# Optimization experiments

Hardware: AMD Instinct MI355X
Metric: run time of the kernel (lower is better)

The kernel has to match this reference:

```python
import jax, jax.numpy as jnp
import numpy as np

N = 80000      # points (voxels)
M = 2048       # windows
C = 128        # d_model
H = 8          # heads
D = C // H     # head_dim = 16
B = 2          # batch size
HB, WB = 32, 32  # BEV window grid shape


def setup_inputs() -> dict:
    key = jax.random.key(0)
    k1, k2, k3, k4 = jax.random.split(key, 4)
    x = jax.random.normal(k1, (N, C), dtype=jnp.float32)
    Wqkv = jax.random.normal(k2, (3 * C, C), dtype=jnp.float32) * 0.05
    Wproj = jax.random.normal(k3, (C, C), dtype=jnp.float32) * 0.05
    bproj = jax.random.normal(k4, (C,), dtype=jnp.float32) * 0.05
    # ragged windows: near-equal contiguous split of N into M groups
    base = N // M
    rem = N - base * M
    counts_np = base + (np.arange(M) < rem).astype(np.int64)
    offsets_np = np.concatenate([[0], np.cumsum(counts_np)[:-1]]).astype(np.int64)
    batch_win_inds_np = np.repeat(np.arange(M, dtype=np.int64), counts_np)
    wid = np.arange(M, dtype=np.int64)
    coords_np = np.stack([wid // (HB * WB), (wid % (HB * WB)) // WB, wid % WB], axis=1)
    return {
        "x": x, "Wqkv": Wqkv, "Wproj": Wproj, "bproj": bproj,
        "offsets": jnp.asarray(offsets_np), "counts": jnp.asarray(counts_np),
        "batch_win_inds": jnp.asarray(batch_win_inds_np),
        "batch_win_coords": jnp.asarray(coords_np),
    }


def _pool3x3(feat, coords):
    # sparse 3x3 sum-pool (stride 1, pad 1) over BEV grid, via dense scatter + shifted sums
    F_ = feat.shape[-1]
    grid = jnp.zeros((B, HB, WB, F_), feat.dtype).at[coords[:, 0], coords[:, 1], coords[:, 2]].set(feat)
    p = jnp.pad(grid, ((0, 0), (1, 1), (1, 1), (0, 0)))
    pooled = sum(p[:, dy:dy + HB, dx:dx + WB] for dy in range(3) for dx in range(3))
    return pooled[coords[:, 0], coords[:, 1], coords[:, 2]]


def reference(x, Wqkv, Wproj, bproj, offsets, counts, batch_win_inds, batch_win_coords):
    n = x.shape[0]
    qkv = (x @ Wqkv.T).reshape(n, 3, H, D)
    q = jax.nn.relu(qkv[:, 0])  # [N, H, D]
    k = jax.nn.relu(qkv[:, 1])
    v = qkv[:, 2]
    # per-window cumulative K^T V (scatter_matmul_kv): [M, H, D, D]
    kv_pt = jnp.einsum('nhd,nhe->nhde', k, v)
    kv = jax.ops.segment_sum(kv_pt, batch_win_inds, num_segments=M)
    # per-window key sum: [M, H, D]
    s = jax.ops.segment_sum(k, batch_win_inds, num_segments=M)
    # 3x3 sum pool over neighboring windows
    kv = _pool3x3(kv.reshape(M, H * D * D), batch_win_coords).reshape(M, H, D, D)
    s = _pool3x3(s.reshape(M, H * D), batch_win_coords).reshape(M, H, D)
    # Q @ C readout (scatter_matmul_qc)
    y = jnp.einsum('nhd,nhde->nhe', q, kv[batch_win_inds])
    z = jnp.sum(s[batch_win_inds] * q, axis=-1, keepdims=True)
    y = y / (z + 1e-6)
    y = y.reshape(n, C)
    return y @ Wproj.T + bproj
```

## Files before the change

kernel.cpp:

```cpp
#include <hip/hip_runtime.h>

#define MWIN 2048
#define HH 8

typedef _Float16 half8 __attribute__((ext_vector_type(8)));
typedef _Float16 half4 __attribute__((ext_vector_type(4)));
typedef float f32x4 __attribute__((ext_vector_type(4)));

__device__ __forceinline__ int win_swz(int bid) {
    return (bid & 7) * 256 + (bid >> 3);
}

__global__ __launch_bounds__(256) void k_prep_w(const float* __restrict__ Wqkv,
                                                const float* __restrict__ Wproj,
                                                _Float16* __restrict__ fq,
                                                _Float16* __restrict__ fp) {
    int tid = blockIdx.x * 256 + threadIdx.x;
    const float* src;
    _Float16* dst;
    if (tid < 6144) { src = Wqkv; dst = fq; }
    else {
        tid -= 6144;
        if (tid >= 2048) return;
        src = Wproj; dst = fp;
    }
    int lane = tid & 63, r = tid >> 6;
    int ct = r & 3, ks = (r >> 2) & 3, cg = r >> 4;
    int m = lane & 15, q = lane >> 4;
    const float* s_ = src + (size_t)(cg * 64 + ct * 16 + m) * 128 + q * 8 + ks * 32;
    float4 f0 = *(const float4*)s_;
    float4 f1 = *(const float4*)(s_ + 4);
    half8 h;
    h[0] = (_Float16)f0.x; h[1] = (_Float16)f0.y; h[2] = (_Float16)f0.z; h[3] = (_Float16)f0.w;
    h[4] = (_Float16)f1.x; h[5] = (_Float16)f1.y; h[6] = (_Float16)f1.z; h[7] = (_Float16)f1.w;
    *(half8*)(dst + (size_t)tid * 8) = h;
}

__global__ __launch_bounds__(512) void k_qkv_win(const float* __restrict__ x,
                                                 const half8* __restrict__ fq,
                                                 const int* __restrict__ offsets,
                                                 const int* __restrict__ counts,
                                                 _Float16* __restrict__ q_h,
                                                 float* __restrict__ kv_t,
                                                 float* __restrict__ s) {
    __shared__ __attribute__((aligned(16))) _Float16 ubuf[18432];
    __shared__ __attribute__((aligned(16))) _Float16 q_lds[48][136];
    _Float16 (*kT)[16][72] = (_Float16(*)[16][72])ubuf;
    _Float16 (*vT)[16][72] = (_Float16(*)[16][72])(ubuf + 9216);

    int w = win_swz(blockIdx.x);
    int off = offsets[w], cnt = counts[w];
    int tid = threadIdx.x;

    #pragma unroll
    for (int it = 0; it < 3; ++it) {
        int j = it * 512 + tid;
        int row = j >> 5, c4 = j & 31;
        int sr = row < cnt ? row : cnt - 1;
        float4 f = *(const float4*)(x + (size_t)(off + sr) * 128 + c4 * 4);
        half4 hv;
        hv[0] = (_Float16)f.x; hv[1] = (_Float16)f.y;
        hv[2] = (_Float16)f.z; hv[3] = (_Float16)f.w;
        *(half4*)&ubuf[row * 136 + c4 * 4] = hv;
    }
    __syncthreads();

    int h = tid >> 6, lane = tid & 63;
    int m = lane & 15, q = lane >> 4;

    half8 a[3][4];
    #pragma unroll
    for (int rt = 0; rt < 3; ++rt)
        #pragma unroll
        for (int ks = 0; ks < 4; ++ks)
            a[rt][ks] = *(const half8*)&ubuf[(rt * 16 + m) * 136 + q * 8 + ks * 32];
    __syncthreads();

    {
        int zh = tid >> 6, zd = (tid >> 2) & 15, zp = 48 + (tid & 3) * 4;
        *(half4*)&kT[zh][zd][zp] = (half4){};
        *(half4*)&vT[zh][zd][zp] = (half4){};
    }

    #pragma unroll
    for (int j = 0; j < 3; ++j) {
        int ctg = h * 3 + j;
        int cg = ctg >> 2, ctl = ctg & 3;
        half8 bfr[4];
        #pragma unroll
        for (int ks = 0; ks < 4; ++ks)
            bfr[ks] = fq[((size_t)cg * 16 + ks * 4 + ctl) * 64 + lane];
        #pragma unroll
        for (int rt = 0; rt < 3; ++rt) {
            f32x4 acc = {};
            #pragma unroll
            for (int ks = 0; ks < 4; ++ks)
                acc = __builtin_amdgcn_mfma_f32_16x16x32_f16(a[rt][ks], bfr[ks], acc, 0, 0, 0);
            int p0 = rt * 16 + q * 4;
            if (ctg < 8) {
                #pragma unroll
                for (int reg = 0; reg < 4; ++reg)
                    q_lds[p0 + reg][ctg * 16 + m] = (_Float16)fmaxf(acc[reg], 0.f);
            } else if (ctg < 16) {
                int head = ctg - 8;
                half4 hv;
                #pragma unroll
                for (int reg = 0; reg < 4; ++reg)
                    hv[reg] = (_Float16)((p0 + reg < cnt) ? fmaxf(acc[reg], 0.f) : 0.f);
                *(half4*)&kT[head][m][p0] = hv;
            } else {
                int head = ctg - 16;
                half4 hv;
                #pragma unroll
                for (int reg = 0; reg < 4; ++reg) hv[reg] = (_Float16)acc[reg];
                *(half4*)&vT[head][m][p0] = hv;
            }
        }
    }
    __syncthreads();

    #pragma unroll
    for (int it = 0; it < 2; ++it) {
        int idx = it * 512 + tid;
        int row = idx >> 4, c8 = idx & 15;
        if (row < cnt)
            *(half8*)(q_h + (size_t)(off + row) * 128 + c8 * 8) = *(const half8*)&q_lds[row][c8 * 8];
    }

    half8 a1 = *(const half8*)&kT[h][m][q * 8];
    half8 a2 = *(const half8*)&kT[h][m][32 + q * 8];
    half8 b1 = *(const half8*)&vT[h][m][q * 8];
    half8 b2 = *(const half8*)&vT[h][m][32 + q * 8];
    half8 ones;
    #pragma unroll
    for (int i = 0; i < 8; ++i) ones[i] = (_Float16)1.0f;
    f32x4 kva = {};
    kva = __builtin_amdgcn_mfma_f32_16x16x32_f16(a1, b1, kva, 0, 0, 0);
    kva = __builtin_amdgcn_mfma_f32_16x16x32_f16(a2, b2, kva, 0, 0, 0);
    f32x4 sa4 = {};
    sa4 = __builtin_amdgcn_mfma_f32_16x16x32_f16(a1, ones, sa4, 0, 0, 0);
    sa4 = __builtin_amdgcn_mfma_f32_16x16x32_f16(a2, ones, sa4, 0, 0, 0);
    *(f32x4*)(kv_t + (((size_t)(w * HH + h)) << 8) + m * 16 + q * 4) = kva;
    if (m == 0)
        *(f32x4*)(s + (((size_t)(w * HH + h)) << 4) + q * 4) = sa4;
}

__global__ __launch_bounds__(512) void k_attn_proj(const _Float16* __restrict__ q_h,
                                                   const float* __restrict__ kv_t,
                                                   const float* __restrict__ s,
                                                   const half8* __restrict__ fp,
                                                   const float* __restrict__ bproj,
                                                   const int* __restrict__ offsets,
                                                   const int* __restrict__ counts,
                                                   float* __restrict__ out) {
    __shared__ _Float16 q_s[48][136];
    __shared__ _Float16 y_t[48][136];
    __shared__ float o_t[16][132];
    int w = win_swz(blockIdx.x);
    int h = threadIdx.x >> 6;
    int lane = threadIdx.x & 63;
    int col = lane & 15;
    int kq = lane >> 4;
    int off = offsets[w], cnt = counts[w];
    bool klive = kq < 2;
    int koff = (kq & 1) * 8;
    int tid = threadIdx.x;

    #pragma unroll
    for (int it = 0; it < 2; ++it) {
        int j = it * 512 + tid;
        int row = j >> 4, c8 = j & 15;
        if (row < 48) {
            int sr = row < cnt ? row : cnt - 1;
            *(half8*)&q_s[row][c8 * 8] =
                *(const half8*)(q_h + (size_t)(off + sr) * 128 + c8 * 8);
        }
    }

    int b = w >> 10, yy = (w >> 5) & 31, xx = w & 31;
    f32x4 k0 = {}, k1 = {}, s0 = {}, s1 = {};
    if (klive) {
        #pragma unroll
        for (int dy = -1; dy <= 1; ++dy)
            #pragma unroll
            for (int dx = -1; dx <= 1; ++dx) {
                int ny = yy + dy, nx = xx + dx;
                if (ny < 0 || ny >= 32 || nx < 0 || nx >= 32) continue;
                int nw = (b << 10) | (ny << 5) | nx;
                const float* kb = kv_t + (((size_t)(nw * HH + h)) << 8) + col * 16 + koff;
                k0 += *(const f32x4*)kb;
                k1 += *(const f32x4*)(kb + 4);
                const float* sb = s + (((size_t)(nw * HH + h)) << 4) + koff;
                s0 += *(const f32x4*)sb;
                s1 += *(const f32x4*)(sb + 4);
            }
    }
    half8 a_kv, a_s;
    #pragma unroll
    for (int i = 0; i < 4; ++i) {
        a_kv[i] = (_Float16)k0[i]; a_kv[4 + i] = (_Float16)k1[i];
        a_s[i]  = (_Float16)s0[i]; a_s[4 + i]  = (_Float16)s1[i];
    }
    __syncthreads();

    #pragma unroll
    for (int c = 0; c < 3; ++c) {
        int p = c * 16 + col;
        half8 b_q = *(const half8*)&q_s[p][h * 16 + koff];
        f32x4 acc = {};
        acc = __builtin_amdgcn_mfma_f32_16x16x32_f16(a_kv, b_q, acc, 0, 0, 0);
        f32x4 accs = {};
        accs = __builtin_amdgcn_mfma_f32_16x16x32_f16(a_s, b_q, accs, 0, 0, 0);
        float zinv = 1.f / (accs[0] + 1e-6f);
        half4 yo;
        #pragma unroll
        for (int i = 0; i < 4; ++i) yo[i] = (_Float16)(acc[i] * zinv);
        *(half4*)&y_t[p][h * 16 + kq * 4] = yo;
    }
    __syncthreads();

    int m = col, q = kq;
    int cg = h >> 2, ctl = h & 3;
    half8 bfr[4];
    #pragma unroll
    for (int ks = 0; ks < 4; ++ks)
        bfr[ks] = fp[((size_t)cg * 16 + ks * 4 + ctl) * 64 + lane];
    float bv = bproj[h * 16 + m];
    #pragma unroll
    for (int rt = 0; rt < 3; ++rt) {
        f32x4 acc = (f32x4){bv, bv, bv, bv};
        #pragma unroll
        for (int ks = 0; ks < 4; ++ks) {
            half8 af = *(const half8*)&y_t[rt * 16 + m][q * 8 + ks * 32];
            acc = __builtin_amdgcn_mfma_f32_16x16x32_f16(af, bfr[ks], acc, 0, 0, 0);
        }
        #pragma unroll
        for (int reg = 0; reg < 4; ++reg)
            o_t[q * 4 + reg][h * 16 + m] = acc[reg];
        __syncthreads();
        int r = tid >> 5, c4 = tid & 31;
        int grow = rt * 16 + r;
        if (grow < cnt)
            *(float4*)(out + ((size_t)(off + grow) << 7) + c4 * 4) = *(const float4*)&o_t[r][c4 * 4];
        __syncthreads();
    }
}

extern "C" void kernel_launch(void* const* d_in, const int* in_sizes, int n_in,
                              void* d_out, int out_size, void* d_ws, size_t ws_size,
                              hipStream_t stream) {
    const float* x     = (const float*)d_in[0];
    const float* Wqkv  = (const float*)d_in[1];
    const float* Wproj = (const float*)d_in[2];
    const float* bproj = (const float*)d_in[3];
    const int*   offsets = (const int*)d_in[4];
    const int*   counts  = (const int*)d_in[5];

    int N = in_sizes[0] / 128;

    char* ws = (char*)d_ws;
    float* kv_t = (float*)ws;                                    ws += (size_t)MWIN * HH * 256 * 4;
    float* s    = (float*)ws;                                    ws += (size_t)MWIN * HH * 16 * 4;
    _Float16* q_h    = (_Float16*)ws;                            ws += (size_t)N * 128 * 2;
    _Float16* fq     = (_Float16*)ws;                            ws += (size_t)6144 * 8 * 2;
    _Float16* fp     = (_Float16*)ws;                            ws += (size_t)2048 * 8 * 2;
    float* out  = (float*)d_out;

    k_prep_w<<<32, 256, 0, stream>>>(Wqkv, Wproj, fq, fp);

    k_qkv_win<<<MWIN, 512, 0, stream>>>(x, (const half8*)fq, offsets, counts,
                                        q_h, kv_t, s);

    k_attn_proj<<<MWIN, 512, 0, stream>>>(q_h, kv_t, s, (const half8*)fp, bproj,
                                          offsets, counts, out);
}
```

Baseline: 145.4 us.

## Alias Q staging onto shared x buffer and reorder QKV tiles per head

Removes the separate q_lds shared array by aliasing it onto the x staging buffer, which cuts LDS per block. Each wave now computes its own head's Q, K and V tiles in sequence (ctg = j*8+h) with the B fragment loaded once per k-step. Q is written out to global before K/V overwrite the buffer, and launch_bounds now requests higher occupancy. This adds two extra block barriers inside the j==0 branch and may raise register pressure from three live accumulators.

```diff
diff --git a/kernel.cpp b/kernel.cpp
--- a/kernel.cpp
+++ b/kernel.cpp
@@ -36,15 +36,16 @@
     *(half8*)(dst + (size_t)tid * 8) = h;
 }
 
-__global__ __launch_bounds__(512) void k_qkv_win(const float* __restrict__ x,
-                                                 const half8* __restrict__ fq,
-                                                 const int* __restrict__ offsets,
-                                                 const int* __restrict__ counts,
-                                                 _Float16* __restrict__ q_h,
-                                                 float* __restrict__ kv_t,
-                                                 float* __restrict__ s) {
+__global__ __launch_bounds__(512, 8) void k_qkv_win(const float* __restrict__ x,
+                                                    const half8* __restrict__ fq,
+                                                    const int* __restrict__ offsets,
+                                                    const int* __restrict__ counts,
+                                                    _Float16* __restrict__ q_h,
+                                                    float* __restrict__ kv_t,
+                                                    float* __restrict__ s) {
     __shared__ __attribute__((aligned(16))) _Float16 ubuf[18432];
-    __shared__ __attribute__((aligned(16))) _Float16 q_lds[48][136];
+    _Float16 (*xs)[136]    = (_Float16(*)[136])ubuf;
+    _Float16 (*q_lds)[136] = (_Float16(*)[136])ubuf;
     _Float16 (*kT)[16][72] = (_Float16(*)[16][72])ubuf;
     _Float16 (*vT)[16][72] = (_Float16(*)[16][72])(ubuf + 9216);
 
@@ -61,7 +62,7 @@
         half4 hv;
         hv[0] = (_Float16)f.x; hv[1] = (_Float16)f.y;
         hv[2] = (_Float16)f.z; hv[3] = (_Float16)f.w;
-        *(half4*)&ubuf[row * 136 + c4 * 4] = hv;
+        *(half4*)&xs[row][c4 * 4] = hv;
     }
     __syncthreads();
 
@@ -73,58 +74,68 @@
     for (int rt = 0; rt < 3; ++rt)
         #pragma unroll
         for (int ks = 0; ks < 4; ++ks)
-            a[rt][ks] = *(const half8*)&ubuf[(rt * 16 + m) * 136 + q * 8 + ks * 32];
-    __syncthreads();
-
-    {
-        int zh = tid >> 6, zd = (tid >> 2) & 15, zp = 48 + (tid & 3) * 4;
-        *(half4*)&kT[zh][zd][zp] = (half4){};
-        *(half4*)&vT[zh][zd][zp] = (half4){};
-    }
+            a[rt][ks] = *(const half8*)&xs[rt * 16 + m][q * 8 + ks * 32];
+    __syncthreads();
 
     #pragma unroll
     for (int j = 0; j < 3; ++j) {
-        int ctg = h * 3 + j;
+        int ctg = j * 8 + h;
         int cg = ctg >> 2, ctl = ctg & 3;
-        half8 bfr[4];
-        #pragma unroll
-        for (int ks = 0; ks < 4; ++ks)
-            bfr[ks] = fq[((size_t)cg * 16 + ks * 4 + ctl) * 64 + lane];
-        #pragma unroll
-        for (int rt = 0; rt < 3; ++rt) {
-            f32x4 acc = {};
-            #pragma unroll
-            for (int ks = 0; ks < 4; ++ks)
-                acc = __builtin_amdgcn_mfma_f32_16x16x32_f16(a[rt][ks], bfr[ks], acc, 0, 0, 0);
-            int p0 = rt * 16 + q * 4;
-            if (ctg < 8) {
-                #pragma unroll
-                for (int reg = 0; reg < 4; ++reg)
-                    q_lds[p0 + reg][ctg * 16 + m] = (_Float16)fmaxf(acc[reg], 0.f);
-            } else if (ctg < 16) {
-                int head = ctg - 8;
+        f32x4 acc0 = {}, acc1 = {}, acc2 = {};
+        #pragma unroll
+        for (int ks = 0; ks < 4; ++ks) {
+            half8 bfr = fq[((size_t)cg * 16 + ks * 4 + ctl) * 64 + lane];
+            acc0 = __builtin_amdgcn_mfma_f32_16x16x32_f16(a[0][ks], bfr, acc0, 0, 0, 0);
+            acc1 = __builtin_amdgcn_mfma_f32_16x16x32_f16(a[1][ks], bfr, acc1, 0, 0, 0);
+            acc2 = __builtin_amdgcn_mfma_f32_16x16x32_f16(a[2][ks], bfr, acc2, 0, 0, 0);
+        }
+        if (j == 0) {
+            #pragma unroll
+            for (int reg = 0; reg < 4; ++reg) {
+                q_lds[q * 4 + reg][h * 16 + m]      = (_Float16)fmaxf(acc0[reg], 0.f);
+                q_lds[16 + q * 4 + reg][h * 16 + m] = (_Float16)fmaxf(acc1[reg], 0.f);
+                q_lds[32 + q * 4 + reg][h * 16 + m] = (_Float16)fmaxf(acc2[reg], 0.f);
+            }
+            __syncthreads();
+            #pragma unroll
+            for (int it = 0; it < 2; ++it) {
+                int idx = it * 512 + tid;
+                int row = idx >> 4, c8 = idx & 15;
+                if (row < cnt)
+                    *(half8*)(q_h + (size_t)(off + row) * 128 + c8 * 8) =
+                        *(const half8*)&q_lds[row][c8 * 8];
+            }
+            __syncthreads();
+        } else if (j == 1) {
+            #pragma unroll
+            for (int rt = 0; rt < 3; ++rt) {
+                f32x4 acc = rt == 0 ? acc0 : (rt == 1 ? acc1 : acc2);
+                int p0 = rt * 16 + q * 4;
                 half4 hv;
                 #pragma unroll
                 for (int reg = 0; reg < 4; ++reg)
                     hv[reg] = (_Float16)((p0 + reg < cnt) ? fmaxf(acc[reg], 0.f) : 0.f);
-                *(half4*)&kT[head][m][p0] = hv;
-            } else {
-                int head = ctg - 16;
+                *(half4*)&kT[h][m][p0] = hv;
+            }
+            {
+                int zd = lane >> 2, zp = 48 + (lane & 3) * 4;
+                *(half4*)&kT[h][zd][zp] = (half4){};
+            }
+        } else {
+            #pragma unroll
+            for (int rt = 0; rt < 3; ++rt) {
+                f32x4 acc = rt == 0 ? acc0 : (rt == 1 ? acc1 : acc2);
+                int p0 = rt * 16 + q * 4;
                 half4 hv;
                 #pragma unroll
                 for (int reg = 0; reg < 4; ++reg) hv[reg] = (_Float16)acc[reg];
-                *(half4*)&vT[head][m][p0] = hv;
-            }
-        }
-    }
-    __syncthreads();
-
-    #pragma unroll
-    for (int it = 0; it < 2; ++it) {
-        int idx = it * 512 + tid;
-        int row = idx >> 4, c8 = idx & 15;
-        if (row < cnt)
-            *(half8*)(q_h + (size_t)(off + row) * 128 + c8 * 8) = *(const half8*)&q_lds[row][c8 * 8];
+                *(half4*)&vT[h][m][p0] = hv;
+            }
+            {
+                int zd = lane >> 2, zp = 48 + (lane & 3) * 4;
+                *(half4*)&vT[h][zd][zp] = (half4){};
+            }
+        }
     }
 
     half8 a1 = *(const half8*)&kT[h][m][q * 8];
```

Result: slower. 215.4 us (+48.1%).
